# Kernel optimization log

Hardware: AMD Instinct MI355X
Metric: run time of the kernel (lower is better)

The kernel has to match this reference:

```python
import jax, jax.numpy as jnp
import numpy as np

B, C, H, W = 16, 256, 64, 64
DIM = 8
HEADS = C // DIM          # 32
TD = HEADS * DIM          # 256 (total_dim)
EPS = 1e-15
BN_EPS = 1e-5


def setup_inputs() -> dict:
    key = jax.random.key(0)
    ks = jax.random.split(key, 7)
    s = 0.05
    return {
        "x": jax.random.normal(ks[0], (B, C, H, W), jnp.float32),
        "w_qkv": jax.random.normal(ks[1], (3 * TD, C), jnp.float32) * s,
        "w_dw": jax.random.normal(ks[2], (3 * TD, 1, 5, 5), jnp.float32) * s,
        "w_pw": jax.random.normal(ks[3], (3 * TD, DIM), jnp.float32) * s,
        "w_proj": jax.random.normal(ks[4], (C, 2 * TD), jnp.float32) * s,
        "bn_gamma": jnp.ones((C,), jnp.float32),
        "bn_beta": jnp.zeros((C,), jnp.float32),
        "bn_mean": jax.random.normal(ks[5], (C,), jnp.float32) * 0.1,
        "bn_var": jax.random.uniform(ks[6], (C,), jnp.float32, 0.5, 1.5),
    }


def reference(x, w_qkv, w_dw, w_pw, w_proj, bn_gamma, bn_beta, bn_mean, bn_var):
    # qkv: 1x1 conv, no bias -> (B, 3*TD, H, W)
    qkv = jnp.einsum('bchw,oc->bohw', x, w_qkv)

    # multi-scale aggregation: 5x5 depthwise conv then grouped 1x1 conv (groups = 3*HEADS)
    dw = jax.lax.conv_general_dilated(
        qkv, w_dw, window_strides=(1, 1), padding=[(2, 2), (2, 2)],
        dimension_numbers=('NCHW', 'OIHW', 'NCHW'), feature_group_count=3 * TD)
    G = 3 * HEADS                                   # groups; DIM channels per group
    dwg = dw.reshape(B, G, DIM, H, W)
    wg = w_pw.reshape(G, DIM, DIM)                  # (group, out_per_group, in_per_group)
    agg = jnp.einsum('bgihw,goi->bgohw', dwg, wg).reshape(B, 3 * TD, H, W)

    qkv_ms = jnp.concatenate([qkv, agg], axis=1)    # (B, 6*TD, H, W)

    # ReLU linear attention (H*W > dim branch)
    h2 = qkv_ms.shape[1] // (3 * DIM)               # 2*HEADS effective heads
    t = qkv_ms.reshape(B, h2, 3 * DIM, H * W)
    q = jax.nn.relu(t[:, :, :DIM])                  # (B,h2,DIM,N)
    k = jax.nn.relu(t[:, :, DIM:2 * DIM])           # (B,h2,DIM,N)
    v = t[:, :, 2 * DIM:]                           # (B,h2,DIM,N)
    v = jnp.concatenate([v, jnp.ones_like(v[:, :, :1])], axis=2)  # pad ones row -> (B,h2,DIM+1,N)

    vk = jnp.einsum('bhen,bhdn->bhed', v, k)        # (B,h2,DIM+1,DIM)
    out = jnp.einsum('bhed,bhdn->bhen', vk, q)      # (B,h2,DIM+1,N)
    out = out[:, :, :-1] / (out[:, :, -1:] + EPS)   # normalize by padded-ones channel
    out = out.reshape(B, h2 * DIM, H, W)            # (B, 2*TD, H, W)

    # proj: 1x1 conv + BatchNorm (inference stats)
    y = jnp.einsum('bchw,oc->bohw', out, w_proj)
    scale = (bn_gamma / jnp.sqrt(bn_var + BN_EPS))[None, :, None, None]
    y = (y - bn_mean[None, :, None, None]) * scale + bn_beta[None, :, None, None]

    return x + y
```

## Files before the change

kernel.cpp:

```cpp
#include <hip/hip_runtime.h>

#define BB 16
#define CC 256
#define HW 4096
#define TD3 768
#define TD2 512
#define WQ_N (TD3 * CC)
#define WP_N (CC * TD2)

typedef __bf16 bf16x8 __attribute__((ext_vector_type(8)));
typedef float f32x4 __attribute__((ext_vector_type(4)));

__device__ inline ushort f2bf(float f) {
    union { float f; uint u; } v; v.f = f;
    uint u = v.u;
    return (ushort)((u + 0x7FFFu + ((u >> 16) & 1u)) >> 16);
}
__device__ inline float bf2f(ushort h) {
    union { uint u; float f; } v; v.u = ((uint)h) << 16;
    return v.f;
}
__device__ inline uint pack2(float a, float b) {
    return (uint)f2bf(a) | ((uint)f2bf(b) << 16);
}

__launch_bounds__(256)
__global__ void k_prep(const float* __restrict__ w_qkv, const float* __restrict__ w_proj,
                       ushort* __restrict__ wq_hi, ushort* __restrict__ wq_lo,
                       ushort* __restrict__ wp_hi, ushort* __restrict__ wp_lo) {
    int i = blockIdx.x * 256 + threadIdx.x;
    if (i < WQ_N) {
        float f = w_qkv[i];
        ushort h = f2bf(f);
        wq_hi[i] = h;
        wq_lo[i] = f2bf(f - bf2f(h));
    }
    if (i < WP_N) {
        float f = w_proj[i];
        ushort h = f2bf(f);
        wp_hi[i] = h;
        wp_lo[i] = f2bf(f - bf2f(h));
    }
}

__launch_bounds__(256)
__global__ void k0_transpose(const float* __restrict__ x, ushort* __restrict__ x_cl) {
    __shared__ float tile[64][65];
    int b = blockIdx.z;
    int n0 = blockIdx.x * 64;
    int c0 = blockIdx.y * 64;
    int t = threadIdx.x;
    const float* xp = x + ((size_t)b * CC + c0) * HW + n0;
    int nl = t & 63;
    int cl0 = t >> 6;
#pragma unroll
    for (int i = 0; i < 16; i++) {
        int cl = cl0 + i * 4;
        tile[cl][nl] = xp[(size_t)cl * HW + nl];
    }
    __syncthreads();
#pragma unroll
    for (int it = 0; it < 2; it++) {
        int item = t + it * 256;
        int n = item >> 3;
        int cc = item & 7;
        uint4 o;
        o.x = pack2(tile[cc * 8 + 0][n], tile[cc * 8 + 1][n]);
        o.y = pack2(tile[cc * 8 + 2][n], tile[cc * 8 + 3][n]);
        o.z = pack2(tile[cc * 8 + 4][n], tile[cc * 8 + 5][n]);
        o.w = pack2(tile[cc * 8 + 6][n], tile[cc * 8 + 7][n]);
        *(uint4*)(x_cl + ((size_t)b * HW + n0 + n) * CC + c0 + cc * 8) = o;
    }
}

__launch_bounds__(256)
__global__ void k1_qkv(const ushort* __restrict__ x_cl, const ushort* __restrict__ wq_hi,
                       const ushort* __restrict__ wq_lo, float* __restrict__ qkv_pl) {
    __shared__ ushort Ald[128][40];
    __shared__ ushort Bh[128][40];
    __shared__ ushort Bl[128][40];
    int b = blockIdx.z;
    int n0 = blockIdx.x * 128;
    int o0 = blockIdx.y * 128;
    int t = threadIdx.x;
    int w = t >> 6, l = t & 63;
    int wn = (w >> 1) * 64, wo = (w & 1) * 64;
    f32x4 acc[4][4];
#pragma unroll
    for (int m = 0; m < 4; m++)
#pragma unroll
        for (int o = 0; o < 4; o++)
#pragma unroll
            for (int r = 0; r < 4; r++) acc[m][o][r] = 0.f;

    const ushort* Ap  = x_cl + ((size_t)b * HW + n0) * CC;
    const ushort* Bph = wq_hi + (size_t)o0 * CC;
    const ushort* Bpl = wq_lo + (size_t)o0 * CC;

    for (int k0 = 0; k0 < CC; k0 += 32) {
#pragma unroll
        for (int it = 0; it < 2; it++) {
            int id = t + it * 256;
            int r = id >> 2, q = id & 3;
            *(uint4*)&Ald[r][q * 8] = *(const uint4*)(Ap + (size_t)r * CC + k0 + q * 8);
        }
#pragma unroll
        for (int it = 0; it < 2; it++) {
            int id = t + it * 256;
            int r = id >> 2, q = id & 3;
            *(uint4*)&Bh[r][q * 8] = *(const uint4*)(Bph + (size_t)r * CC + k0 + q * 8);
            *(uint4*)&Bl[r][q * 8] = *(const uint4*)(Bpl + (size_t)r * CC + k0 + q * 8);
        }
        __syncthreads();
        bf16x8 af[4], bh[4], bl[4];
#pragma unroll
        for (int m = 0; m < 4; m++) af[m] = *(const bf16x8*)&Ald[wn + m * 16 + (l & 15)][(l >> 4) * 8];
#pragma unroll
        for (int o = 0; o < 4; o++) {
            bh[o] = *(const bf16x8*)&Bh[wo + o * 16 + (l & 15)][(l >> 4) * 8];
            bl[o] = *(const bf16x8*)&Bl[wo + o * 16 + (l & 15)][(l >> 4) * 8];
        }
#pragma unroll
        for (int m = 0; m < 4; m++)
#pragma unroll
            for (int o = 0; o < 4; o++) {
                acc[m][o] = __builtin_amdgcn_mfma_f32_16x16x32_bf16(af[m], bh[o], acc[m][o], 0, 0, 0);
                acc[m][o] = __builtin_amdgcn_mfma_f32_16x16x32_bf16(af[m], bl[o], acc[m][o], 0, 0, 0);
            }
        __syncthreads();
    }
#pragma unroll
    for (int m = 0; m < 4; m++) {
        int nb = n0 + wn + m * 16 + (l >> 4) * 4;
#pragma unroll
        for (int oi = 0; oi < 4; oi++) {
            int o = o0 + wo + oi * 16 + (l & 15);
            float4 v4 = {acc[m][oi][0], acc[m][oi][1], acc[m][oi][2], acc[m][oi][3]};
            *(float4*)(qkv_pl + ((size_t)b * TD3 + o) * HW + nb) = v4;
        }
    }
}

__launch_bounds__(256)
__global__ void k2_dwpw(const float* __restrict__ qkv_pl, const float* __restrict__ w_dw,
                        const float* __restrict__ w_pw, float* __restrict__ agg_pl) {
    __shared__ __align__(16) float lds[2][36][76];
    int g = blockIdx.x;
    int strip = blockIdx.y;
    int b = blockIdx.z;
    int t = threadIdx.x;
    int y0 = strip * 32;
    const float* wg  = w_dw + (size_t)g * 200;
    const float* wpg = w_pw + (size_t)g * 64;
    const float* src = qkv_pl + ((size_t)b * TD3 + g * 8) * HW;
    float* dst = agg_pl + ((size_t)b * TD3 + g * 8) * HW;

    int rp = t >> 4;
    int seg = t & 15;

    float ag[8][8];
#pragma unroll
    for (int o = 0; o < 8; o++)
#pragma unroll
        for (int j = 0; j < 8; j++) ag[o][j] = 0.f;

#pragma unroll 1
    for (int cp = 0; cp < 4; cp++) {
        if (cp) __syncthreads();
        if (cp == 0) {
            if (t < 144) {
                int ch = t / 72, rem = t - ch * 72;
                int row = rem >> 1, side = rem & 1;
                float2 z2 = {0.f, 0.f};
                *(float2*)(&lds[ch][row][side ? 66 : 0]) = z2;
            }
        }
#pragma unroll
        for (int i = 0; i < 5; i++) {
            int slot = t + i * 256;
            if (slot < 1152) {
                int ch = slot / 576;
                int rem = slot - ch * 576;
                int row = rem >> 4;
                int q = rem & 15;
                int yy = y0 - 2 + row;
                float4 v = {0.f, 0.f, 0.f, 0.f};
                if (yy >= 0 && yy < 64)
                    v = *(const float4*)(src + (size_t)(2 * cp + ch) * HW + yy * 64 + q * 4);
                float2 lo2 = {v.x, v.y}, hi2 = {v.z, v.w};
                *(float2*)(&lds[ch][row][2 + 4 * q]) = lo2;
                *(float2*)(&lds[ch][row][4 + 4 * q]) = hi2;
            }
        }
        __syncthreads();
#pragma unroll
        for (int ch = 0; ch < 2; ch++) {
            int c = cp * 2 + ch;
            float dw0[4] = {0.f, 0.f, 0.f, 0.f};
            float dw1[4] = {0.f, 0.f, 0.f, 0.f};
#pragma unroll
            for (int j = 0; j < 6; j++) {
                float win[8];
                *(float4*)&win[0] = *(const float4*)&lds[ch][rp * 2 + j][4 * seg];
                *(float4*)&win[4] = *(const float4*)&lds[ch][rp * 2 + j][4 * seg + 4];
                if (j <= 4) {
#pragma unroll
                    for (int dx = 0; dx < 5; dx++) {
                        float wv = wg[c * 25 + j * 5 + dx];
#pragma unroll
                        for (int k = 0; k < 4; k++) dw0[k] += win[dx + k] * wv;
                    }
                }
                if (j >= 1) {
#pragma unroll
                    for (int dx = 0; dx < 5; dx++) {
                        float wv = wg[c * 25 + (j - 1) * 5 + dx];
#pragma unroll
                        for (int k = 0; k < 4; k++) dw1[k] += win[dx + k] * wv;
                    }
                }
            }
#pragma unroll
            for (int o = 0; o < 8; o++) {
                float wv = wpg[o * 8 + c];
#pragma unroll
                for (int k = 0; k < 4; k++) {
                    ag[o][k] += dw0[k] * wv;
                    ag[o][4 + k] += dw1[k] * wv;
                }
            }
        }
    }
    int n0 = (y0 + rp * 2) * 64 + seg * 4;
#pragma unroll
    for (int o = 0; o < 8; o++) {
        float4 r0 = {ag[o][0], ag[o][1], ag[o][2], ag[o][3]};
        float4 r1 = {ag[o][4], ag[o][5], ag[o][6], ag[o][7]};
        *(float4*)(dst + (size_t)o * HW + n0) = r0;
        *(float4*)(dst + (size_t)o * HW + n0 + 64) = r1;
    }
}

__launch_bounds__(256)
__global__ void k3_vk(const float* __restrict__ qkv_pl, const float* __restrict__ agg_pl,
                      float* __restrict__ vk_buf) {
    __shared__ float vk_partial[4][72];
    int h = blockIdx.x;
    int b = blockIdx.y;
    int s = blockIdx.z;
    const float* src = (h < 32) ? (qkv_pl + ((size_t)b * TD3 + h * 24) * HW)
                                : (agg_pl + ((size_t)b * TD3 + (h - 32) * 24) * HW);
    const float* kp = src + (size_t)8 * HW;
    const float* vp = src + (size_t)16 * HW;
    int t = threadIdx.x;
    float vk[9][8];
#pragma unroll
    for (int e = 0; e < 9; e++)
#pragma unroll
        for (int d = 0; d < 8; d++) vk[e][d] = 0.f;

#pragma unroll
    for (int it = 0; it < 2; it++) {
        int n4 = s * 2048 + (t + it * 256) * 4;
        float4 kf[8], vf[8];
#pragma unroll
        for (int d = 0; d < 8; d++) kf[d] = *(const float4*)(kp + (size_t)d * HW + n4);
#pragma unroll
        for (int e = 0; e < 8; e++) vf[e] = *(const float4*)(vp + (size_t)e * HW + n4);
#pragma unroll
        for (int d = 0; d < 8; d++) {
            kf[d].x = fmaxf(kf[d].x, 0.f); kf[d].y = fmaxf(kf[d].y, 0.f);
            kf[d].z = fmaxf(kf[d].z, 0.f); kf[d].w = fmaxf(kf[d].w, 0.f);
        }
#pragma unroll
        for (int e = 0; e < 8; e++)
#pragma unroll
            for (int d = 0; d < 8; d++)
                vk[e][d] += vf[e].x * kf[d].x + vf[e].y * kf[d].y + vf[e].z * kf[d].z + vf[e].w * kf[d].w;
#pragma unroll
        for (int d = 0; d < 8; d++) vk[8][d] += kf[d].x + kf[d].y + kf[d].z + kf[d].w;
    }
#pragma unroll
    for (int e = 0; e < 9; e++)
#pragma unroll
        for (int d = 0; d < 8; d++) {
            float v = vk[e][d];
            for (int off = 32; off > 0; off >>= 1) v += __shfl_xor(v, off);
            vk[e][d] = v;
        }
    int w = t >> 6, l = t & 63;
    if (l == 0) {
#pragma unroll
        for (int e = 0; e < 9; e++)
#pragma unroll
            for (int d = 0; d < 8; d++) vk_partial[w][e * 8 + d] = vk[e][d];
    }
    __syncthreads();
    if (t < 72) {
        float sum = vk_partial[0][t] + vk_partial[1][t] + vk_partial[2][t] + vk_partial[3][t];
        vk_buf[(((size_t)b * 64 + h) * 2 + s) * 72 + t] = sum;
    }
}

__launch_bounds__(256)
__global__ void k3_out(const float* __restrict__ qkv_pl, const float* __restrict__ agg_pl,
                       const float* __restrict__ vk_buf, ushort* __restrict__ out_cl) {
    __shared__ float vk_s[72];
    int h = blockIdx.x;
    int b = blockIdx.y;
    int s = blockIdx.z;
    const float* src = (h < 32) ? (qkv_pl + ((size_t)b * TD3 + h * 24) * HW)
                                : (agg_pl + ((size_t)b * TD3 + (h - 32) * 24) * HW);
    int t = threadIdx.x;
    if (t < 72) {
        const float* vb = vk_buf + ((size_t)b * 64 + h) * 2 * 72 + t;
        vk_s[t] = vb[0] + vb[72];
    }
    __syncthreads();
    float vkf[9][8];
#pragma unroll
    for (int e = 0; e < 9; e++)
#pragma unroll
        for (int d = 0; d < 8; d++) vkf[e][d] = vk_s[e * 8 + d];

    int n4 = s * 1024 + t * 4;
    float qa[4][8];
#pragma unroll
    for (int d = 0; d < 8; d++) {
        float4 q4 = *(const float4*)(src + (size_t)d * HW + n4);
        qa[0][d] = fmaxf(q4.x, 0.f); qa[1][d] = fmaxf(q4.y, 0.f);
        qa[2][d] = fmaxf(q4.z, 0.f); qa[3][d] = fmaxf(q4.w, 0.f);
    }
    ushort* dst = out_cl + (size_t)b * HW * TD2 + h * 8;
#pragma unroll
    for (int j = 0; j < 4; j++) {
        float o[9];
#pragma unroll
        for (int e = 0; e < 9; e++) {
            float sum = 0.f;
#pragma unroll
            for (int d = 0; d < 8; d++) sum += vkf[e][d] * qa[j][d];
            o[e] = sum;
        }
        float inv = 1.f / (o[8] + 1e-15f);
        uint4 ov;
        ov.x = pack2(o[0] * inv, o[1] * inv); ov.y = pack2(o[2] * inv, o[3] * inv);
        ov.z = pack2(o[4] * inv, o[5] * inv); ov.w = pack2(o[6] * inv, o[7] * inv);
        *(uint4*)(dst + (size_t)(n4 + j) * TD2) = ov;
    }
}

__launch_bounds__(256)
__global__ void k4_proj(const ushort* __restrict__ out_cl, const ushort* __restrict__ wp_hi,
                        const ushort* __restrict__ wp_lo, const float* __restrict__ x,
                        const float* __restrict__ gamma, const float* __restrict__ beta,
                        const float* __restrict__ mean, const float* __restrict__ var_,
                        float* __restrict__ out) {
    __shared__ ushort Ah[128][40];
    __shared__ ushort Al[128][40];
    __shared__ ushort Bld[128][40];
    int b = blockIdx.z;
    int n0 = blockIdx.x * 128;
    int c0 = blockIdx.y * 128;
    int t = threadIdx.x;
    int w = t >> 6, l = t & 63;
    int wc = (w >> 1) * 64, wn = (w & 1) * 64;
    f32x4 acc[4][4];
#pragma unroll
    for (int m = 0; m < 4; m++)
#pragma unroll
        for (int o = 0; o < 4; o++)
#pragma unroll
            for (int r = 0; r < 4; r++) acc[m][o][r] = 0.f;

    const ushort* Aph = wp_hi + (size_t)c0 * TD2;
    const ushort* Apl = wp_lo + (size_t)c0 * TD2;
    const ushort* Bp  = out_cl + ((size_t)b * HW + n0) * TD2;

    for (int k0 = 0; k0 < TD2; k0 += 32) {
#pragma unroll
        for (int it = 0; it < 2; it++) {
            int id = t + it * 256;
            int r = id >> 2, q = id & 3;
            *(uint4*)&Ah[r][q * 8] = *(const uint4*)(Aph + (size_t)r * TD2 + k0 + q * 8);
            *(uint4*)&Al[r][q * 8] = *(const uint4*)(Apl + (size_t)r * TD2 + k0 + q * 8);
        }
#pragma unroll
        for (int it = 0; it < 2; it++) {
            int id = t + it * 256;
            int r = id >> 2, q = id & 3;
            *(uint4*)&Bld[r][q * 8] = *(const uint4*)(Bp + (size_t)r * TD2 + k0 + q * 8);
        }
        __syncthreads();
        bf16x8 ah[4], al[4], bf[4];
#pragma unroll
        for (int m = 0; m < 4; m++) {
            ah[m] = *(const bf16x8*)&Ah[wc + m * 16 + (l & 15)][(l >> 4) * 8];
            al[m] = *(const bf16x8*)&Al[wc + m * 16 + (l & 15)][(l >> 4) * 8];
        }
#pragma unroll
        for (int ni = 0; ni < 4; ni++) bf[ni] = *(const bf16x8*)&Bld[wn + ni * 16 + (l & 15)][(l >> 4) * 8];
#pragma unroll
        for (int m = 0; m < 4; m++)
#pragma unroll
            for (int ni = 0; ni < 4; ni++) {
                acc[m][ni] = __builtin_amdgcn_mfma_f32_16x16x32_bf16(ah[m], bf[ni], acc[m][ni], 0, 0, 0);
                acc[m][ni] = __builtin_amdgcn_mfma_f32_16x16x32_bf16(al[m], bf[ni], acc[m][ni], 0, 0, 0);
            }
        __syncthreads();
    }
#pragma unroll
    for (int m = 0; m < 4; m++) {
        int cb = c0 + wc + m * 16 + (l >> 4) * 4;
        float sc[4], mn[4], bt[4];
#pragma unroll
        for (int r = 0; r < 4; r++) {
            sc[r] = gamma[cb + r] * rsqrtf(var_[cb + r] + 1e-5f);
            mn[r] = mean[cb + r];
            bt[r] = beta[cb + r];
        }
#pragma unroll
        for (int ni = 0; ni < 4; ni++) {
            int n = n0 + wn + ni * 16 + (l & 15);
#pragma unroll
            for (int r = 0; r < 4; r++) {
                size_t idx = ((size_t)b * CC + cb + r) * HW + n;
                out[idx] = x[idx] + (acc[m][ni][r] - mn[r]) * sc[r] + bt[r];
            }
        }
    }
}

extern "C" void kernel_launch(void* const* d_in, const int* in_sizes, int n_in,
                              void* d_out, int out_size, void* d_ws, size_t ws_size,
                              hipStream_t stream) {
    const float* x      = (const float*)d_in[0];
    const float* w_qkv  = (const float*)d_in[1];
    const float* w_dw   = (const float*)d_in[2];
    const float* w_pw   = (const float*)d_in[3];
    const float* w_proj = (const float*)d_in[4];
    const float* gamma  = (const float*)d_in[5];
    const float* beta   = (const float*)d_in[6];
    const float* mean   = (const float*)d_in[7];
    const float* var_   = (const float*)d_in[8];
    float* out = (float*)d_out;

    const size_t static_bytes = ((size_t)WQ_N + WP_N) * 2 * 2;
    const size_t per_batch = (size_t)HW * CC * 2 + (size_t)HW * TD3 * 4 * 2 + (size_t)HW * TD2 * 2
                           + (size_t)64 * 2 * 72 * 4;
    size_t avail = ws_size > static_bytes ? ws_size - static_bytes : 0;
    int cb = 16;
    while (cb > 1 && (size_t)cb * per_batch > avail) cb >>= 1;

    char* ws = (char*)d_ws;
    ushort* x_cl   = (ushort*)ws;
    float*  qkv_pl = (float*)(ws + (size_t)cb * HW * CC * 2);
    float*  agg_pl = (float*)(ws + (size_t)cb * HW * CC * 2 + (size_t)cb * HW * TD3 * 4);
    ushort* out_cl = (ushort*)(ws + (size_t)cb * HW * CC * 2 + (size_t)cb * HW * TD3 * 8);
    float*  vk_buf = (float*)(ws + (size_t)cb * HW * CC * 2 + (size_t)cb * HW * TD3 * 8
                                 + (size_t)cb * HW * TD2 * 2);
    char* wsw = ws + (size_t)cb * per_batch;
    ushort* wq_hi = (ushort*)wsw;
    ushort* wq_lo = wq_hi + WQ_N;
    ushort* wp_hi = wq_lo + WQ_N;
    ushort* wp_lo = wp_hi + WP_N;

    k_prep<<<dim3((WQ_N + 255) / 256), 256, 0, stream>>>(w_qkv, w_proj, wq_hi, wq_lo, wp_hi, wp_lo);

    for (int b0 = 0; b0 < BB; b0 += cb) {
        const float* xc = x + (size_t)b0 * CC * HW;
        float* oc = out + (size_t)b0 * CC * HW;
        k0_transpose<<<dim3(64, 4, cb), 256, 0, stream>>>(xc, x_cl);
        k1_qkv<<<dim3(32, 6, cb), 256, 0, stream>>>(x_cl, wq_hi, wq_lo, qkv_pl);
        k2_dwpw<<<dim3(96, 2, cb), 256, 0, stream>>>(qkv_pl, w_dw, w_pw, agg_pl);
        k3_vk<<<dim3(64, cb, 2), 256, 0, stream>>>(qkv_pl, agg_pl, vk_buf);
        k3_out<<<dim3(64, cb, 4), 256, 0, stream>>>(qkv_pl, agg_pl, vk_buf, out_cl);
        k4_proj<<<dim3(32, 2, cb), 256, 0, stream>>>(out_cl, wp_hi, wp_lo, xc, gamma, beta, mean, var_, oc);
    }
}
```

Baseline: 415.4 us.

## Use direct global-to-LDS loads in GEMMs and prefetch depthwise conv input

The two bf16 GEMM kernels now stage their tiles with global_load_lds (direct global-to-LDS DMA, 16 bytes per lane) instead of loading into registers and then storing to LDS. This removes the padding so the LDS rows stay contiguous for the DMA layout. The depthwise/pointwise kernel now loads the next channel pair into registers while it computes on the current pair, which overlaps global latency with FMA work. Removing the padding can cause LDS bank conflicts on the MFMA fragment reads, and the prefetch adds register pressure.

```diff
diff --git a/kernel.cpp b/kernel.cpp
--- a/kernel.cpp
+++ b/kernel.cpp
@@ -10,6 +10,8 @@
 
 typedef __bf16 bf16x8 __attribute__((ext_vector_type(8)));
 typedef float f32x4 __attribute__((ext_vector_type(4)));
+typedef const __attribute__((address_space(1))) unsigned int glb_u32;
+typedef __attribute__((address_space(3))) unsigned int lds_u32;
 
 __device__ inline ushort f2bf(float f) {
     union { float f; uint u; } v; v.f = f;
@@ -76,9 +78,9 @@
 __launch_bounds__(256)
 __global__ void k1_qkv(const ushort* __restrict__ x_cl, const ushort* __restrict__ wq_hi,
                        const ushort* __restrict__ wq_lo, float* __restrict__ qkv_pl) {
-    __shared__ ushort Ald[128][40];
-    __shared__ ushort Bh[128][40];
-    __shared__ ushort Bl[128][40];
+    __shared__ ushort Ald[128][32];
+    __shared__ ushort Bh[128][32];
+    __shared__ ushort Bl[128][32];
     int b = blockIdx.z;
     int n0 = blockIdx.x * 128;
     int o0 = blockIdx.y * 128;
@@ -96,20 +98,20 @@
     const ushort* Ap  = x_cl + ((size_t)b * HW + n0) * CC;
     const ushort* Bph = wq_hi + (size_t)o0 * CC;
     const ushort* Bpl = wq_lo + (size_t)o0 * CC;
+    int rowl = (l >> 2);
+    int coll = (l & 3) * 8;
 
     for (int k0 = 0; k0 < CC; k0 += 32) {
 #pragma unroll
-        for (int it = 0; it < 2; it++) {
-            int id = t + it * 256;
-            int r = id >> 2, q = id & 3;
-            *(uint4*)&Ald[r][q * 8] = *(const uint4*)(Ap + (size_t)r * CC + k0 + q * 8);
-        }
-#pragma unroll
-        for (int it = 0; it < 2; it++) {
-            int id = t + it * 256;
-            int r = id >> 2, q = id & 3;
-            *(uint4*)&Bh[r][q * 8] = *(const uint4*)(Bph + (size_t)r * CC + k0 + q * 8);
-            *(uint4*)&Bl[r][q * 8] = *(const uint4*)(Bpl + (size_t)r * CC + k0 + q * 8);
+        for (int i = 0; i < 2; i++) {
+            int rbase = w * 32 + i * 16;
+            int row = rbase + rowl;
+            __builtin_amdgcn_global_load_lds((glb_u32*)(Ap + (size_t)row * CC + k0 + coll),
+                                             (lds_u32*)&Ald[rbase][0], 16, 0, 0);
+            __builtin_amdgcn_global_load_lds((glb_u32*)(Bph + (size_t)row * CC + k0 + coll),
+                                             (lds_u32*)&Bh[rbase][0], 16, 0, 0);
+            __builtin_amdgcn_global_load_lds((glb_u32*)(Bpl + (size_t)row * CC + k0 + coll),
+                                             (lds_u32*)&Bl[rbase][0], 16, 0, 0);
         }
         __syncthreads();
         bf16x8 af[4], bh[4], bl[4];
@@ -158,6 +160,42 @@
     int rp = t >> 4;
     int seg = t & 15;
 
+    int s_ch[5], s_row[5], s_q[5], s_ok[5];
+#pragma unroll
+    for (int i = 0; i < 5; i++) {
+        int slot = t + i * 256;
+        s_ok[i] = slot < 1152;
+        int ch = slot / 576;
+        int rem = slot - ch * 576;
+        s_ch[i] = ch; s_row[i] = rem >> 4; s_q[i] = rem & 15;
+    }
+
+    if (t < 144) {
+        int ch = t / 72, rem = t - ch * 72;
+        int row = rem >> 1, side = rem & 1;
+        float2 z2 = {0.f, 0.f};
+        *(float2*)(&lds[ch][row][side ? 66 : 0]) = z2;
+    }
+
+    float4 sv[5];
+#pragma unroll
+    for (int i = 0; i < 5; i++) {
+        float4 v = {0.f, 0.f, 0.f, 0.f};
+        int yy = y0 - 2 + s_row[i];
+        if (s_ok[i] && yy >= 0 && yy < 64)
+            v = *(const float4*)(src + (size_t)s_ch[i] * HW + yy * 64 + s_q[i] * 4);
+        sv[i] = v;
+    }
+#pragma unroll
+    for (int i = 0; i < 5; i++) {
+        if (s_ok[i]) {
+            float2 lo2 = {sv[i].x, sv[i].y}, hi2 = {sv[i].z, sv[i].w};
+            *(float2*)(&lds[s_ch[i]][s_row[i]][2 + 4 * s_q[i]]) = lo2;
+            *(float2*)(&lds[s_ch[i]][s_row[i]][4 + 4 * s_q[i]]) = hi2;
+        }
+    }
+    __syncthreads();
+
     float ag[8][8];
 #pragma unroll
     for (int o = 0; o < 8; o++)
@@ -166,33 +204,16 @@
 
 #pragma unroll 1
     for (int cp = 0; cp < 4; cp++) {
-        if (cp) __syncthreads();
-        if (cp == 0) {
-            if (t < 144) {
-                int ch = t / 72, rem = t - ch * 72;
-                int row = rem >> 1, side = rem & 1;
-                float2 z2 = {0.f, 0.f};
-                *(float2*)(&lds[ch][row][side ? 66 : 0]) = z2;
-            }
-        }
-#pragma unroll
-        for (int i = 0; i < 5; i++) {
-            int slot = t + i * 256;
-            if (slot < 1152) {
-                int ch = slot / 576;
-                int rem = slot - ch * 576;
-                int row = rem >> 4;
-                int q = rem & 15;
-                int yy = y0 - 2 + row;
+        if (cp < 3) {
+#pragma unroll
+            for (int i = 0; i < 5; i++) {
                 float4 v = {0.f, 0.f, 0.f, 0.f};
-                if (yy >= 0 && yy < 64)
-                    v = *(const float4*)(src + (size_t)(2 * cp + ch) * HW + yy * 64 + q * 4);
-                float2 lo2 = {v.x, v.y}, hi2 = {v.z, v.w};
-                *(float2*)(&lds[ch][row][2 + 4 * q]) = lo2;
-                *(float2*)(&lds[ch][row][4 + 4 * q]) = hi2;
-            }
-        }
-        __syncthreads();
+                int yy = y0 - 2 + s_row[i];
+                if (s_ok[i] && yy >= 0 && yy < 64)
+                    v = *(const float4*)(src + (size_t)(2 * (cp + 1) + s_ch[i]) * HW + yy * 64 + s_q[i] * 4);
+                sv[i] = v;
+            }
+        }
 #pragma unroll
         for (int ch = 0; ch < 2; ch++) {
             int c = cp * 2 + ch;
@@ -229,6 +250,18 @@
                     ag[o][4 + k] += dw1[k] * wv;
                 }
             }
+        }
+        if (cp < 3) {
+            __syncthreads();
+#pragma unroll
+            for (int i = 0; i < 5; i++) {
+                if (s_ok[i]) {
+                    float2 lo2 = {sv[i].x, sv[i].y}, hi2 = {sv[i].z, sv[i].w};
+                    *(float2*)(&lds[s_ch[i]][s_row[i]][2 + 4 * s_q[i]]) = lo2;
+                    *(float2*)(&lds[s_ch[i]][s_row[i]][4 + 4 * s_q[i]]) = hi2;
+                }
+            }
+            __syncthreads();
         }
     }
     int n0 = (y0 + rp * 2) * 64 + seg * 4;
@@ -356,9 +389,9 @@
                         const float* __restrict__ gamma, const float* __restrict__ beta,
                         const float* __restrict__ mean, const float* __restrict__ var_,
                         float* __restrict__ out) {
-    __shared__ ushort Ah[128][40];
-    __shared__ ushort Al[128][40];
-    __shared__ ushort Bld[128][40];
+    __shared__ ushort Ah[128][32];
+    __shared__ ushort Al[128][32];
+    __shared__ ushort Bld[128][32];
     int b = blockIdx.z;
     int n0 = blockIdx.x * 128;
     int c0 = blockIdx.y * 128;
@@ -376,20 +409,20 @@
     const ushort* Aph = wp_hi + (size_t)c0 * TD2;
     const ushort* Apl = wp_lo + (size_t)c0 * TD2;
     const ushort* Bp  = out_cl + ((size_t)b * HW + n0) * TD2;
+    int rowl = (l >> 2);
+    int coll = (l & 3) * 8;
 
     for (int k0 = 0; k0 < TD2; k0 += 32) {
 #pragma unroll
-        for (int it = 0; it < 2; it++) {
-            int id = t + it * 256;
-            int r = id >> 2, q = id & 3;
-            *(uint4*)&Ah[r][q * 8] = *(const uint4*)(Aph + (size_t)r * TD2 + k0 + q * 8);
-            *(uint4*)&Al[r][q * 8] = *(const uint4*)(Apl + (size_t)r * TD2 + k0 + q * 8);
-        }
-#pragma unroll
-        for (int it = 0; it < 2; it++) {
-            int id = t + it * 256;
-            int r = id >> 2, q = id & 3;
-            *(uint4*)&Bld[r][q * 8] = *(const uint4*)(Bp + (size_t)r * TD2 + k0 + q * 8);
+        for (int i = 0; i < 2; i++) {
+            int rbase = w * 32 + i * 16;
+            int row = rbase + rowl;
+            __builtin_amdgcn_global_load_lds((glb_u32*)(Aph + (size_t)row * TD2 + k0 + coll),
+                                             (lds_u32*)&Ah[rbase][0], 16, 0, 0);
+            __builtin_amdgcn_global_load_lds((glb_u32*)(Apl + (size_t)row * TD2 + k0 + coll),
+                                             (lds_u32*)&Al[rbase][0], 16, 0, 0);
+            __builtin_amdgcn_global_load_lds((glb_u32*)(Bp + (size_t)row * TD2 + k0 + coll),
+                                             (lds_u32*)&Bld[rbase][0], 16, 0, 0);
         }
         __syncthreads();
         bf16x8 ah[4], al[4], bf[4];
```

After: 423.4 us. Within noise of the previous version (+1.9%).
